# Performance work log

Hardware: AMD Instinct MI355X
Metric: run time of the kernel (lower is better)

## Reference

```python
import jax, jax.numpy as jnp
import numpy as np

S, D, P, R, E, M, K = 1024, 1024, 2816, 64, 8, 16, 1


def setup_inputs() -> dict:
    key = jax.random.key(0)
    ks = jax.random.split(key, 10)
    xav_a = (2.0 / (P + R)) ** 0.5   # xavier_uniform-like std for adapters
    xav_d = (2.0 / (D + P)) ** 0.5   # xavier for down projections
    bank_s = (1.0 / D) ** 0.5        # keep basis columns O(1)
    return {
        "hidden_states": jax.random.normal(ks[0], (S, D), jnp.float32),
        "expert_indices": jax.random.randint(ks[1], (S, K), 0, E),
        "expert_weights": jax.random.uniform(ks[2], (S, K), jnp.float32),
        "up_adapters": jax.random.normal(ks[3], (E, P, R), jnp.float32) * xav_a,
        "gate_adapters": jax.random.normal(ks[4], (E, P, R), jnp.float32) * xav_a,
        "up_mixture_logits": jax.random.normal(ks[5], (E, M), jnp.float32) * 0.01,
        "gate_mixture_logits": jax.random.normal(ks[6], (E, M), jnp.float32) * 0.01,
        "down_projections": jax.random.normal(ks[7], (E, D, P), jnp.float32) * xav_d,
        "up_bank": jax.random.normal(ks[8], (M, D, R), jnp.float32) * bank_s,
        "gate_bank": jax.random.normal(ks[9], (M, D, R), jnp.float32) * bank_s,
    }


def reference(hidden_states, expert_indices, expert_weights,
              up_adapters, gate_adapters, up_mixture_logits,
              gate_mixture_logits, down_projections, up_bank, gate_bank):
    n_experts = down_projections.shape[0]
    # SparseMixer: token-independent mixture weights over global bases (softmax)
    alpha_up = jax.nn.softmax(up_mixture_logits, axis=-1)      # [E, M]
    alpha_gate = jax.nn.softmax(gate_mixture_logits, axis=-1)  # [E, M]
    # Compose per-expert mixed bases: sum_j alpha_{e,j} B_j -> [E, D, R]
    up_mixed = jnp.einsum('em,mdr->edr', alpha_up, up_bank)
    gate_mixed = jnp.einsum('em,mdr->edr', alpha_gate, gate_bank)
    # Recomposed Up/Gate weights: A_e @ mixed_e^T -> [E, P, D]
    W_up = jnp.einsum('epr,edr->epd', up_adapters, up_mixed)
    W_gate = jnp.einsum('epr,edr->epd', gate_adapters, gate_mixed)
    # Combine routing weights per (token, expert): sum over topk slots
    onehot = (expert_indices[..., None] == jnp.arange(n_experts)).astype(hidden_states.dtype)  # [S,K,E]
    comb = jnp.einsum('ske,sk->se', onehot, expert_weights)  # [S, E]
    out = jnp.zeros_like(hidden_states)
    for e in range(n_experts):  # fixed small expert count
        up = hidden_states @ W_up[e].T        # [S, P]
        gate = hidden_states @ W_gate[e].T    # [S, P]
        inter = jax.nn.silu(gate) * up        # gated activation
        out = out + (inter @ down_projections[e].T) * comb[:, e:e + 1]
    return out
```

## Files before the change

### kernel.cpp

```cpp
#include <hip/hip_runtime.h>
#include <hip/hip_bf16.h>
#include <math.h>

#define S 1024
#define D 1024
#define P 2816
#define R 64
#define E 8
#define M 16
#define DSPLIT 8
#define KSPLIT 4
#define KQ (P / KSPLIT)
#define NIT (KQ / 64)

typedef __attribute__((ext_vector_type(8))) short short8;
typedef __attribute__((ext_vector_type(4))) float floatx4;

static __device__ inline unsigned short f2bf(float f) {
  __hip_bfloat16 h = __float2bfloat16(f);
  return *reinterpret_cast<unsigned short*>(&h);
}

__global__ __launch_bounds__(256) void k_pre(
    const float* __restrict__ up_logits, const float* __restrict__ gate_logits,
    const float* __restrict__ up_bank, const float* __restrict__ gate_bank,
    const int* __restrict__ idx,
    unsigned short* __restrict__ mxu, unsigned short* __restrict__ mxg,
    int* __restrict__ perm, int* __restrict__ offs, float* __restrict__ out) {
  int b = blockIdx.x, t = threadIdx.x;
  float4 z4 = make_float4(0.f, 0.f, 0.f, 0.f);
#pragma unroll
  for (int j = 0; j < 4; ++j)
    *(float4*)(out + (size_t)b * 4096 + j * 1024 + t * 4) = z4;

  if (b == 0) {
    __shared__ int hist[E];
    __shared__ int basearr[E];
    if (t < E) hist[t] = 0;
    __syncthreads();
    int e4[4];
#pragma unroll
    for (int j = 0; j < 4; ++j) {
      e4[j] = idx[t + j * 256];
      atomicAdd(&hist[e4[j]], 1);
    }
    __syncthreads();
    if (t == 0) {
      int run = 0;
      for (int i = 0; i < E; ++i) { basearr[i] = run; offs[i] = run; run += hist[i]; }
      offs[E] = S;
    }
    __syncthreads();
#pragma unroll
    for (int j = 0; j < 4; ++j) {
      int pos = atomicAdd(&basearr[e4[j]], 1);
      perm[pos] = t + j * 256;
    }
  }

  __shared__ float alpha[2][E][M];
  if (t < 16) {
    int mat = t >> 3, e = t & 7;
    const float* lg = (mat ? gate_logits : up_logits) + e * M;
    float v[M], mx = -1e30f, s = 0.f;
#pragma unroll
    for (int m = 0; m < M; ++m) { v[m] = lg[m]; mx = fmaxf(mx, v[m]); }
#pragma unroll
    for (int m = 0; m < M; ++m) { v[m] = expf(v[m] - mx); s += v[m]; }
#pragma unroll
    for (int m = 0; m < M; ++m) alpha[mat][e][m] = v[m] / s;
  }
  __syncthreads();
  int g = b * 256 + t;
  int d = g >> 6, r = g & 63;
  float au[E] = {0, 0, 0, 0, 0, 0, 0, 0}, ag[E] = {0, 0, 0, 0, 0, 0, 0, 0};
#pragma unroll
  for (int m = 0; m < M; ++m) {
    float vu = up_bank[((size_t)m * D + d) * R + r];
    float vg = gate_bank[((size_t)m * D + d) * R + r];
#pragma unroll
    for (int e = 0; e < E; ++e) {
      au[e] += alpha[0][e][m] * vu;
      ag[e] += alpha[1][e][m] * vg;
    }
  }
#pragma unroll
  for (int e = 0; e < E; ++e) {
    mxu[((size_t)e * D + d) * R + r] = f2bf(au[e]);
    mxg[((size_t)e * D + d) * R + r] = f2bf(ag[e]);
  }
}

__global__ __launch_bounds__(256) void k_t(
    const float* __restrict__ H, const unsigned short* __restrict__ mxu,
    const unsigned short* __restrict__ mxg, const int* __restrict__ perm,
    const int* __restrict__ offs, float* __restrict__ tpart) {
  int e = blockIdx.x;
  int start = offs[e] + blockIdx.y * 64;
  int end = offs[e + 1];
  if (start >= end) return;
  int z = blockIdx.z;
  __shared__ unsigned short As[64][72];
  __shared__ unsigned short Bs[128][72];
  int t = threadIdx.x;
  int lane = t & 63, w = t >> 6, quad = lane >> 4, l15 = lane & 15;
  int rows[2];
#pragma unroll
  for (int j = 0; j < 2; ++j) {
    int c = t + j * 256;
    int pos = start + (c >> 3);
    rows[j] = (pos < end) ? perm[pos] : -1;
  }
  floatx4 acc[8];
#pragma unroll
  for (int nt = 0; nt < 8; ++nt) acc[nt] = (floatx4){0.f, 0.f, 0.f, 0.f};

  for (int it = 0; it < 2; ++it) {
    int k0 = z * 128 + it * 64;
#pragma unroll
    for (int j = 0; j < 2; ++j) {
      int c = t + j * 256;
      int arow = c >> 3, acol = (c & 7) * 8;
      short8 v = (short8){0, 0, 0, 0, 0, 0, 0, 0};
      if (rows[j] >= 0) {
        const float* src = H + (size_t)rows[j] * D + k0 + acol;
        float4 f0 = *(const float4*)src;
        float4 f1 = *(const float4*)(src + 4);
        v[0] = f2bf(f0.x); v[1] = f2bf(f0.y); v[2] = f2bf(f0.z); v[3] = f2bf(f0.w);
        v[4] = f2bf(f1.x); v[5] = f2bf(f1.y); v[6] = f2bf(f1.z); v[7] = f2bf(f1.w);
      }
      *(short8*)&As[arow][acol] = v;
    }
    {
      int dd = t >> 2, r0 = (t & 3) * 16;
      const unsigned short* su = mxu + ((size_t)e * D + k0 + dd) * R + r0;
      const unsigned short* sg = mxg + ((size_t)e * D + k0 + dd) * R + r0;
      short8 u0 = *(const short8*)su, u1 = *(const short8*)(su + 8);
      short8 g0 = *(const short8*)sg, g1 = *(const short8*)(sg + 8);
#pragma unroll
      for (int j = 0; j < 8; ++j) {
        Bs[r0 + j][dd] = u0[j];
        Bs[r0 + 8 + j][dd] = u1[j];
        Bs[64 + r0 + j][dd] = g0[j];
        Bs[64 + r0 + 8 + j][dd] = g1[j];
      }
    }
    __syncthreads();
#pragma unroll
    for (int ks = 0; ks < 2; ++ks) {
      int kc = ks * 32 + quad * 8;
      short8 a = *(const short8*)&As[w * 16 + l15][kc];
#pragma unroll
      for (int nt = 0; nt < 8; ++nt) {
        short8 bb = *(const short8*)&Bs[nt * 16 + l15][kc];
        acc[nt] = __builtin_amdgcn_mfma_f32_16x16x32_bf16(a, bb, acc[nt], 0, 0, 0);
      }
    }
    __syncthreads();
  }
#pragma unroll
  for (int reg = 0; reg < 4; ++reg) {
    int pos = start + w * 16 + quad * 4 + reg;
    if (pos < end) {
#pragma unroll
      for (int nt = 0; nt < 8; ++nt)
        tpart[((size_t)z * S + pos) * 128 + nt * 16 + l15] = acc[nt][reg];
    }
  }
}

__global__ __launch_bounds__(256) void k_tred(
    const float* __restrict__ tpart, unsigned short* __restrict__ tbuf) {
  int i = blockIdx.x * 256 + threadIdx.x;
  float s = 0.f;
#pragma unroll
  for (int ds = 0; ds < DSPLIT; ++ds) s += tpart[(size_t)ds * S * 128 + i];
  tbuf[i] = f2bf(s);
}

__global__ __launch_bounds__(256) void k_inter(
    const unsigned short* __restrict__ tbuf, const float* __restrict__ Aup,
    const float* __restrict__ Agate, const int* __restrict__ offs,
    unsigned short* __restrict__ inter) {
  int e = blockIdx.x;
  int start = offs[e] + blockIdx.y * 64;
  int end = offs[e + 1];
  if (start >= end) return;
  int p0 = blockIdx.z * 128;
  __shared__ unsigned short Ts[64][136];
  __shared__ unsigned short Bu[128][72];
  __shared__ unsigned short Bg[128][72];
  int t = threadIdx.x;
  int lane = t & 63, w = t >> 6;
#pragma unroll
  for (int j = 0; j < 4; ++j) {
    int i = t + j * 256;
    int row = i >> 4, c8 = (i & 15) * 8;
    int pos = start + row;
    float4 v = (pos < end) ? *(const float4*)(tbuf + (size_t)pos * 128 + c8)
                           : make_float4(0.f, 0.f, 0.f, 0.f);
    *(float4*)&Ts[row][c8] = v;
  }
#pragma unroll
  for (int j = 0; j < 4; ++j) {
    int i = t + j * 256;
    int pr = i >> 3, c8 = (i & 7) * 8;
    const float* su = Aup + ((size_t)(e * P + p0 + pr) * R + c8);
    const float* sg = Agate + ((size_t)(e * P + p0 + pr) * R + c8);
    float4 u0 = *(const float4*)su, u1 = *(const float4*)(su + 4);
    float4 g0 = *(const float4*)sg, g1 = *(const float4*)(sg + 4);
    short8 uv, gv;
    uv[0] = f2bf(u0.x); uv[1] = f2bf(u0.y); uv[2] = f2bf(u0.z); uv[3] = f2bf(u0.w);
    uv[4] = f2bf(u1.x); uv[5] = f2bf(u1.y); uv[6] = f2bf(u1.z); uv[7] = f2bf(u1.w);
    gv[0] = f2bf(g0.x); gv[1] = f2bf(g0.y); gv[2] = f2bf(g0.z); gv[3] = f2bf(g0.w);
    gv[4] = f2bf(g1.x); gv[5] = f2bf(g1.y); gv[6] = f2bf(g1.z); gv[7] = f2bf(g1.w);
    *(short8*)&Bu[pr][c8] = uv;
    *(short8*)&Bg[pr][c8] = gv;
  }
  __syncthreads();
  int quad = lane >> 4, l15 = lane & 15;
  floatx4 au_acc[4][2], ag_acc[4][2];
#pragma unroll
  for (int tt = 0; tt < 4; ++tt)
#pragma unroll
    for (int pt = 0; pt < 2; ++pt) {
      au_acc[tt][pt] = (floatx4){0.f, 0.f, 0.f, 0.f};
      ag_acc[tt][pt] = (floatx4){0.f, 0.f, 0.f, 0.f};
    }
#pragma unroll
  for (int ks = 0; ks < 2; ++ks) {
    int kc = ks * 32 + quad * 8;
    short8 au[4], ag[4], bu[2], bg[2];
#pragma unroll
    for (int tt = 0; tt < 4; ++tt) {
      au[tt] = *(const short8*)&Ts[tt * 16 + l15][kc];
      ag[tt] = *(const short8*)&Ts[tt * 16 + l15][64 + kc];
    }
#pragma unroll
    for (int pt = 0; pt < 2; ++pt) {
      bu[pt] = *(const short8*)&Bu[w * 32 + pt * 16 + l15][kc];
      bg[pt] = *(const short8*)&Bg[w * 32 + pt * 16 + l15][kc];
    }
#pragma unroll
    for (int tt = 0; tt < 4; ++tt)
#pragma unroll
      for (int pt = 0; pt < 2; ++pt) {
        au_acc[tt][pt] = __builtin_amdgcn_mfma_f32_16x16x32_bf16(au[tt], bu[pt], au_acc[tt][pt], 0, 0, 0);
        ag_acc[tt][pt] = __builtin_amdgcn_mfma_f32_16x16x32_bf16(ag[tt], bg[pt], ag_acc[tt][pt], 0, 0, 0);
      }
  }
#pragma unroll
  for (int tt = 0; tt < 4; ++tt)
#pragma unroll
    for (int reg = 0; reg < 4; ++reg) {
      int row = tt * 16 + quad * 4 + reg;
      int pos = start + row;
      if (pos < end) {
#pragma unroll
        for (int pt = 0; pt < 2; ++pt) {
          float g = ag_acc[tt][pt][reg];
          float u = au_acc[tt][pt][reg];
          float val = u * (g / (1.f + __expf(-g)));
          inter[(size_t)pos * P + p0 + w * 32 + pt * 16 + l15] = f2bf(val);
        }
      }
    }
}

__global__ __launch_bounds__(256) void k_down(
    const unsigned short* __restrict__ inter, const float* __restrict__ Wd,
    const int* __restrict__ perm, const int* __restrict__ offs,
    const float* __restrict__ wts, float* __restrict__ out) {
  int e = blockIdx.x;
  int start = offs[e];
  int end = offs[e + 1];
  if (start >= end) return;
  int kz = blockIdx.y;
  int d0 = blockIdx.z * 64;
  __shared__ unsigned short As[256][72];
  __shared__ unsigned short Bs[64][72];
  int t = threadIdx.x;
  int lane = t & 63, w = t >> 6, quad = lane >> 4, l15 = lane & 15;

  const unsigned short* aptr[8];
  bool aok[8];
#pragma unroll
  for (int j = 0; j < 8; ++j) {
    int arow = (t >> 3) + 32 * j;
    int pos = start + arow;
    aok[j] = (pos < end);
    aptr[j] = inter + (size_t)(aok[j] ? pos : start) * P + kz * KQ + (t & 7) * 8;
  }
  const float* bsrc = Wd + ((size_t)(e * D + d0 + (t >> 2)) * P + kz * KQ + (t & 3) * 16);

  float4 pa[8];
  float4 pb[4];
#pragma unroll
  for (int j = 0; j < 8; ++j)
    pa[j] = aok[j] ? *(const float4*)(aptr[j]) : make_float4(0.f, 0.f, 0.f, 0.f);
#pragma unroll
  for (int q = 0; q < 4; ++q) pb[q] = *(const float4*)(bsrc + q * 4);

  floatx4 acc[4][4];
#pragma unroll
  for (int tt = 0; tt < 4; ++tt)
#pragma unroll
    for (int dt = 0; dt < 4; ++dt) acc[tt][dt] = (floatx4){0.f, 0.f, 0.f, 0.f};

  for (int it = 0; it < NIT; ++it) {
#pragma unroll
    for (int j = 0; j < 8; ++j)
      *(float4*)&As[(t >> 3) + 32 * j][(t & 7) * 8] = pa[j];
    {
      short8 bv0, bv1;
      bv0[0] = f2bf(pb[0].x); bv0[1] = f2bf(pb[0].y); bv0[2] = f2bf(pb[0].z); bv0[3] = f2bf(pb[0].w);
      bv0[4] = f2bf(pb[1].x); bv0[5] = f2bf(pb[1].y); bv0[6] = f2bf(pb[1].z); bv0[7] = f2bf(pb[1].w);
      bv1[0] = f2bf(pb[2].x); bv1[1] = f2bf(pb[2].y); bv1[2] = f2bf(pb[2].z); bv1[3] = f2bf(pb[2].w);
      bv1[4] = f2bf(pb[3].x); bv1[5] = f2bf(pb[3].y); bv1[6] = f2bf(pb[3].z); bv1[7] = f2bf(pb[3].w);
      *(short8*)&Bs[t >> 2][(t & 3) * 16] = bv0;
      *(short8*)&Bs[t >> 2][(t & 3) * 16 + 8] = bv1;
    }
    __syncthreads();
    if (it + 1 < NIT) {
      int k0 = (it + 1) * 64;
#pragma unroll
      for (int j = 0; j < 8; ++j)
        pa[j] = aok[j] ? *(const float4*)(aptr[j] + k0) : make_float4(0.f, 0.f, 0.f, 0.f);
#pragma unroll
      for (int q = 0; q < 4; ++q) pb[q] = *(const float4*)(bsrc + k0 + q * 4);
    }
#pragma unroll
    for (int ks = 0; ks < 2; ++ks) {
      int kc = ks * 32 + quad * 8;
      short8 a[4], b[4];
#pragma unroll
      for (int tt = 0; tt < 4; ++tt) a[tt] = *(const short8*)&As[w * 64 + tt * 16 + l15][kc];
#pragma unroll
      for (int dt = 0; dt < 4; ++dt) b[dt] = *(const short8*)&Bs[dt * 16 + l15][kc];
#pragma unroll
      for (int tt = 0; tt < 4; ++tt)
#pragma unroll
        for (int dt = 0; dt < 4; ++dt)
          acc[tt][dt] = __builtin_amdgcn_mfma_f32_16x16x32_bf16(a[tt], b[dt], acc[tt][dt], 0, 0, 0);
    }
    __syncthreads();
  }
#pragma unroll
  for (int tt = 0; tt < 4; ++tt)
#pragma unroll
    for (int reg = 0; reg < 4; ++reg) {
      int pos = start + w * 64 + tt * 16 + quad * 4 + reg;
      if (pos < end) {
        int tok = perm[pos];
        float wt = wts[tok];
#pragma unroll
        for (int dt = 0; dt < 4; ++dt)
          atomicAdd(&out[(size_t)tok * D + d0 + dt * 16 + l15], acc[tt][dt][reg] * wt);
      }
    }
}

extern "C" void kernel_launch(void* const* d_in, const int* in_sizes, int n_in,
                              void* d_out, int out_size, void* d_ws, size_t ws_size,
                              hipStream_t stream) {
  const float* H = (const float*)d_in[0];
  const int* idx = (const int*)d_in[1];
  const float* wts = (const float*)d_in[2];
  const float* Aup = (const float*)d_in[3];
  const float* Agate = (const float*)d_in[4];
  const float* upl = (const float*)d_in[5];
  const float* gatel = (const float*)d_in[6];
  const float* Wd = (const float*)d_in[7];
  const float* upb = (const float*)d_in[8];
  const float* gateb = (const float*)d_in[9];
  float* out = (float*)d_out;

  char* ws = (char*)d_ws;
  unsigned short* mxu = (unsigned short*)ws;
  unsigned short* mxg = mxu + (size_t)E * D * R;
  float* tpart = (float*)(mxg + (size_t)E * D * R);
  unsigned short* tbuf = (unsigned short*)(tpart + (size_t)DSPLIT * S * 128);
  unsigned short* inter = tbuf + (size_t)S * 128;
  int* perm = (int*)(inter + (size_t)S * P);
  int* offs = perm + S;

  k_pre<<<256, 256, 0, stream>>>(upl, gatel, upb, gateb, idx, mxu, mxg, perm, offs, out);
  k_t<<<dim3(E, 4, DSPLIT), 256, 0, stream>>>(H, mxu, mxg, perm, offs, tpart);
  k_tred<<<512, 256, 0, stream>>>(tpart, tbuf);
  k_inter<<<dim3(E, 4, P / 128), 256, 0, stream>>>(tbuf, Aup, Agate, offs, inter);
  k_down<<<dim3(E, KSPLIT, D / 64), 256, 0, stream>>>(inter, Wd, perm, offs, wts, out);
}
```

Measured before the change: 212.3 us.

## Fuse split-D reduction into k_t via atomics and retile k_inter

k_t now accumulates its split-D partial results straight into an fp32 buffer with atomicAdd. That buffer is zeroed in k_pre, so the separate k_tred reduction kernel and the 8x partial buffer it read are gone. k_inter reads the fp32 buffer and converts it to bf16 while staging it into shared memory. k_inter is also retiled from 64 tokens by 128 P columns to 128 tokens by 64 P columns, which changes how the adapter loads are reused across blocks. The atomics make the summation order nondeterministic and may contend on the shared fp32 buffer.

```diff
diff --git a/kernel.cpp b/kernel.cpp
--- a/kernel.cpp
+++ b/kernel.cpp
@@ -26,12 +26,14 @@
     const float* __restrict__ up_bank, const float* __restrict__ gate_bank,
     const int* __restrict__ idx,
     unsigned short* __restrict__ mxu, unsigned short* __restrict__ mxg,
-    int* __restrict__ perm, int* __restrict__ offs, float* __restrict__ out) {
+    int* __restrict__ perm, int* __restrict__ offs, float* __restrict__ out,
+    float* __restrict__ tbuf32) {
   int b = blockIdx.x, t = threadIdx.x;
   float4 z4 = make_float4(0.f, 0.f, 0.f, 0.f);
 #pragma unroll
   for (int j = 0; j < 4; ++j)
     *(float4*)(out + (size_t)b * 4096 + j * 1024 + t * 4) = z4;
+  *(float2*)(tbuf32 + (size_t)b * 512 + t * 2) = make_float2(0.f, 0.f);
 
   if (b == 0) {
     __shared__ int hist[E];
@@ -94,7 +96,7 @@
 __global__ __launch_bounds__(256) void k_t(
     const float* __restrict__ H, const unsigned short* __restrict__ mxu,
     const unsigned short* __restrict__ mxg, const int* __restrict__ perm,
-    const int* __restrict__ offs, float* __restrict__ tpart) {
+    const int* __restrict__ offs, float* __restrict__ tbuf32) {
   int e = blockIdx.x;
   int start = offs[e] + blockIdx.y * 64;
   int end = offs[e + 1];
@@ -164,45 +166,42 @@
     if (pos < end) {
 #pragma unroll
       for (int nt = 0; nt < 8; ++nt)
-        tpart[((size_t)z * S + pos) * 128 + nt * 16 + l15] = acc[nt][reg];
-    }
-  }
-}
-
-__global__ __launch_bounds__(256) void k_tred(
-    const float* __restrict__ tpart, unsigned short* __restrict__ tbuf) {
-  int i = blockIdx.x * 256 + threadIdx.x;
-  float s = 0.f;
-#pragma unroll
-  for (int ds = 0; ds < DSPLIT; ++ds) s += tpart[(size_t)ds * S * 128 + i];
-  tbuf[i] = f2bf(s);
+        atomicAdd(&tbuf32[(size_t)pos * 128 + nt * 16 + l15], acc[nt][reg]);
+    }
+  }
 }
 
 __global__ __launch_bounds__(256) void k_inter(
-    const unsigned short* __restrict__ tbuf, const float* __restrict__ Aup,
+    const float* __restrict__ tbuf32, const float* __restrict__ Aup,
     const float* __restrict__ Agate, const int* __restrict__ offs,
     unsigned short* __restrict__ inter) {
   int e = blockIdx.x;
-  int start = offs[e] + blockIdx.y * 64;
+  int start = offs[e] + blockIdx.y * 128;
   int end = offs[e + 1];
   if (start >= end) return;
-  int p0 = blockIdx.z * 128;
-  __shared__ unsigned short Ts[64][136];
-  __shared__ unsigned short Bu[128][72];
-  __shared__ unsigned short Bg[128][72];
+  int p0 = blockIdx.z * 64;
+  __shared__ unsigned short Ts[128][136];
+  __shared__ unsigned short Bu[64][72];
+  __shared__ unsigned short Bg[64][72];
   int t = threadIdx.x;
-  int lane = t & 63, w = t >> 6;
-#pragma unroll
-  for (int j = 0; j < 4; ++j) {
+  int lane = t & 63, w = t >> 6, quad = lane >> 4, l15 = lane & 15;
+#pragma unroll
+  for (int j = 0; j < 8; ++j) {
     int i = t + j * 256;
     int row = i >> 4, c8 = (i & 15) * 8;
     int pos = start + row;
-    float4 v = (pos < end) ? *(const float4*)(tbuf + (size_t)pos * 128 + c8)
-                           : make_float4(0.f, 0.f, 0.f, 0.f);
-    *(float4*)&Ts[row][c8] = v;
-  }
-#pragma unroll
-  for (int j = 0; j < 4; ++j) {
+    short8 v = (short8){0, 0, 0, 0, 0, 0, 0, 0};
+    if (pos < end) {
+      const float* src = tbuf32 + (size_t)pos * 128 + c8;
+      float4 f0 = *(const float4*)src;
+      float4 f1 = *(const float4*)(src + 4);
+      v[0] = f2bf(f0.x); v[1] = f2bf(f0.y); v[2] = f2bf(f0.z); v[3] = f2bf(f0.w);
+      v[4] = f2bf(f1.x); v[5] = f2bf(f1.y); v[6] = f2bf(f1.z); v[7] = f2bf(f1.w);
+    }
+    *(short8*)&Ts[row][c8] = v;
+  }
+#pragma unroll
+  for (int j = 0; j < 2; ++j) {
     int i = t + j * 256;
     int pr = i >> 3, c8 = (i & 7) * 8;
     const float* su = Aup + ((size_t)(e * P + p0 + pr) * R + c8);
@@ -218,50 +217,49 @@
     *(short8*)&Bg[pr][c8] = gv;
   }
   __syncthreads();
-  int quad = lane >> 4, l15 = lane & 15;
-  floatx4 au_acc[4][2], ag_acc[4][2];
-#pragma unroll
-  for (int tt = 0; tt < 4; ++tt)
-#pragma unroll
-    for (int pt = 0; pt < 2; ++pt) {
+  floatx4 au_acc[2][4], ag_acc[2][4];
+#pragma unroll
+  for (int tt = 0; tt < 2; ++tt)
+#pragma unroll
+    for (int pt = 0; pt < 4; ++pt) {
       au_acc[tt][pt] = (floatx4){0.f, 0.f, 0.f, 0.f};
       ag_acc[tt][pt] = (floatx4){0.f, 0.f, 0.f, 0.f};
     }
 #pragma unroll
-  for (int ks = 0; ks < 2; ++ks) {
-    int kc = ks * 32 + quad * 8;
-    short8 au[4], ag[4], bu[2], bg[2];
-#pragma unroll
-    for (int tt = 0; tt < 4; ++tt) {
-      au[tt] = *(const short8*)&Ts[tt * 16 + l15][kc];
-      ag[tt] = *(const short8*)&Ts[tt * 16 + l15][64 + kc];
-    }
-#pragma unroll
-    for (int pt = 0; pt < 2; ++pt) {
-      bu[pt] = *(const short8*)&Bu[w * 32 + pt * 16 + l15][kc];
-      bg[pt] = *(const short8*)&Bg[w * 32 + pt * 16 + l15][kc];
-    }
-#pragma unroll
-    for (int tt = 0; tt < 4; ++tt)
-#pragma unroll
-      for (int pt = 0; pt < 2; ++pt) {
+  for (int kh = 0; kh < 2; ++kh) {
+    int kc = kh * 32 + quad * 8;
+    short8 au[2], ag[2], bu[4], bg[4];
+#pragma unroll
+    for (int tt = 0; tt < 2; ++tt) {
+      au[tt] = *(const short8*)&Ts[w * 32 + tt * 16 + l15][kc];
+      ag[tt] = *(const short8*)&Ts[w * 32 + tt * 16 + l15][64 + kc];
+    }
+#pragma unroll
+    for (int pt = 0; pt < 4; ++pt) {
+      bu[pt] = *(const short8*)&Bu[pt * 16 + l15][kc];
+      bg[pt] = *(const short8*)&Bg[pt * 16 + l15][kc];
+    }
+#pragma unroll
+    for (int tt = 0; tt < 2; ++tt)
+#pragma unroll
+      for (int pt = 0; pt < 4; ++pt) {
         au_acc[tt][pt] = __builtin_amdgcn_mfma_f32_16x16x32_bf16(au[tt], bu[pt], au_acc[tt][pt], 0, 0, 0);
         ag_acc[tt][pt] = __builtin_amdgcn_mfma_f32_16x16x32_bf16(ag[tt], bg[pt], ag_acc[tt][pt], 0, 0, 0);
       }
   }
 #pragma unroll
-  for (int tt = 0; tt < 4; ++tt)
+  for (int tt = 0; tt < 2; ++tt)
 #pragma unroll
     for (int reg = 0; reg < 4; ++reg) {
-      int row = tt * 16 + quad * 4 + reg;
+      int row = w * 32 + tt * 16 + quad * 4 + reg;
       int pos = start + row;
       if (pos < end) {
 #pragma unroll
-        for (int pt = 0; pt < 2; ++pt) {
+        for (int pt = 0; pt < 4; ++pt) {
           float g = ag_acc[tt][pt][reg];
           float u = au_acc[tt][pt][reg];
           float val = u * (g / (1.f + __expf(-g)));
-          inter[(size_t)pos * P + p0 + w * 32 + pt * 16 + l15] = f2bf(val);
+          inter[(size_t)pos * P + p0 + pt * 16 + l15] = f2bf(val);
         }
       }
     }
@@ -378,15 +376,13 @@
   char* ws = (char*)d_ws;
   unsigned short* mxu = (unsigned short*)ws;
   unsigned short* mxg = mxu + (size_t)E * D * R;
-  float* tpart = (float*)(mxg + (size_t)E * D * R);
-  unsigned short* tbuf = (unsigned short*)(tpart + (size_t)DSPLIT * S * 128);
-  unsigned short* inter = tbuf + (size_t)S * 128;
+  float* tbuf32 = (float*)(mxg + (size_t)E * D * R);
+  unsigned short* inter = (unsigned short*)(tbuf32 + (size_t)S * 128);
   int* perm = (int*)(inter + (size_t)S * P);
   int* offs = perm + S;
 
-  k_pre<<<256, 256, 0, stream>>>(upl, gatel, upb, gateb, idx, mxu, mxg, perm, offs, out);
-  k_t<<<dim3(E, 4, DSPLIT), 256, 0, stream>>>(H, mxu, mxg, perm, offs, tpart);
-  k_tred<<<512, 256, 0, stream>>>(tpart, tbuf);
-  k_inter<<<dim3(E, 4, P / 128), 256, 0, stream>>>(tbuf, Aup, Agate, offs, inter);
+  k_pre<<<256, 256, 0, stream>>>(upl, gatel, upb, gateb, idx, mxu, mxg, perm, offs, out, tbuf32);
+  k_t<<<dim3(E, 4, DSPLIT), 256, 0, stream>>>(H, mxu, mxg, perm, offs, tbuf32);
+  k_inter<<<dim3(E, 2, P / 64), 256, 0, stream>>>(tbuf32, Aup, Agate, offs, inter);
   k_down<<<dim3(E, KSPLIT, D / 64), 256, 0, stream>>>(inter, Wd, perm, offs, wts, out);
 }
```

Result: no change. 213.0 us (+0.3%).
